# Optimization experiments

Hardware: AMD Instinct MI355X
Metric: run time of the kernel (lower is better)

Reference implementation:

```python
import jax, jax.numpy as jnp
import numpy as np

B, NQ, NK, QS, KS, H, VD = 16, 64, 512, 256, 256, 256, 256


def setup_inputs() -> dict:
    key = jax.random.key(0)
    k1, k2, k3, k4, k5, k6, k7 = jax.random.split(key, 7)
    return {
        "queries": jax.random.normal(k1, (B, NQ, QS), dtype=jnp.float32),
        "keys": jax.random.normal(k2, (B, NK, KS), dtype=jnp.float32),
        "values": jax.random.normal(k3, (B, NK, VD), dtype=jnp.float32),
        "valid_lens": jax.random.randint(k4, (B,), 1, NK + 1, dtype=jnp.int32),
        # learned params (nn.Linear with bias=False): W_q [QS,H], W_k [KS,H], w_v [H]
        "W_q": jax.random.normal(k5, (QS, H), dtype=jnp.float32) / np.sqrt(QS),
        "W_k": jax.random.normal(k6, (KS, H), dtype=jnp.float32) / np.sqrt(KS),
        "w_v": jax.random.normal(k7, (H,), dtype=jnp.float32) / np.sqrt(H),
    }


def reference(queries, keys, values, valid_lens, W_q, W_k, w_v):
    # project: q [B,nq,H], k [B,nk,H]
    q = jnp.einsum("bqd,dh->bqh", queries, W_q)
    k = jnp.einsum("bkd,dh->bkh", keys, W_k)
    # broadcast-add -> tanh -> score reduction via w_v: [B,nq,nk]
    features = jnp.tanh(q[:, :, None, :] + k[:, None, :, :])  # [B,nq,nk,H]
    scores = jnp.einsum("bqkh,h->bqk", features, w_v)
    # masked softmax over keys (positions >= valid_len masked out)
    mask = jnp.arange(scores.shape[-1])[None, None, :] < valid_lens[:, None, None]
    scores = jnp.where(mask, scores, -1e6)
    attn = jax.nn.softmax(scores, axis=-1)
    # weighted sum of values (dropout p=0 / eval mode => identity)
    return jnp.einsum("bqk,bkv->bqv", attn, values)
```

## Files before the change

### kernel.cpp

```cpp
#include <hip/hip_runtime.h>
#include <hip/hip_bf16.h>

#define BB 16
#define NQ 64
#define NK 512
#define HD 256

typedef __attribute__((ext_vector_type(8))) short short8;
typedef __attribute__((ext_vector_type(4))) float f32x4;

__device__ __forceinline__ ushort bf16_rne(float v) {
    unsigned u = __float_as_uint(v);
    return (ushort)((u + 0x7FFFu + ((u >> 16) & 1u)) >> 16);
}
__device__ __forceinline__ float bf16_to_f(ushort h) {
    return __uint_as_float(((unsigned)h) << 16);
}

__global__ __launch_bounds__(256) void wconv(
    const float* __restrict__ wq, const float* __restrict__ wk,
    ushort* __restrict__ wqh, ushort* __restrict__ wql,
    ushort* __restrict__ wkh, ushort* __restrict__ wkl)
{
    int widx = blockIdx.x * 256 + threadIdx.x;
    const float* W; ushort *wh, *wl;
    if (widx < 16384) { W = wq; wh = wqh; wl = wql; }
    else { W = wk; wh = wkh; wl = wkl; widx -= 16384; }
    int n  = widx >> 6;
    int k4 = (widx & 63) * 4;
    ushort hh[4], ll[4];
    #pragma unroll
    for (int c = 0; c < 4; ++c) {
        float v = W[(k4 + c) * 256 + n];
        hh[c] = bf16_rne(v);
        ll[c] = bf16_rne(v - bf16_to_f(hh[c]));
    }
    *(ushort4*)&wh[n * 256 + k4] = make_ushort4(hh[0], hh[1], hh[2], hh[3]);
    *(ushort4*)&wl[n * 256 + k4] = make_ushort4(ll[0], ll[1], ll[2], ll[3]);
}

__global__ __launch_bounds__(256, 2) void proj_fused(
    const float* __restrict__ queries, const float* __restrict__ keys,
    const ushort* __restrict__ wqh, const ushort* __restrict__ wql,
    const ushort* __restrict__ wkh, const ushort* __restrict__ wkl,
    float* __restrict__ qp, float* __restrict__ kp, float scale)
{
    __shared__ ushort AsH[64 * 64], AsL[64 * 64];
    __shared__ ushort BsH[64 * 64], BsL[64 * 64];

    const float* A; const ushort *Bh, *Bl; float* C; int rows0;
    const int bx = blockIdx.x;
    if (bx < 16) { A = queries; Bh = wqh; Bl = wql; C = qp; rows0 = bx * 64; }
    else         { A = keys;    Bh = wkh; Bl = wkl; C = kp; rows0 = (bx - 16) * 64; }
    const int cols0 = blockIdx.y * 64;

    const int t = threadIdx.x, lane = t & 63, wave = t >> 6;
    const int quad = lane >> 4, l15 = lane & 15;
    const int sr  = t >> 2;
    const int sc2 = (t & 3) * 2;

    f32x4 acc[4];
    #pragma unroll
    for (int j = 0; j < 4; ++j) acc[j] = (f32x4){0.f, 0.f, 0.f, 0.f};

    for (int k0 = 0; k0 < 256; k0 += 64) {
        const float* arow = &A[(size_t)(rows0 + sr) * 256 + k0 + sc2 * 8];
        float4 a0 = *(const float4*)&arow[0];
        float4 a1 = *(const float4*)&arow[4];
        float4 a2 = *(const float4*)&arow[8];
        float4 a3 = *(const float4*)&arow[12];
        const ushort* bhp = &Bh[(size_t)(cols0 + sr) * 256 + k0 + sc2 * 8];
        const ushort* blp = &Bl[(size_t)(cols0 + sr) * 256 + k0 + sc2 * 8];
        short8 b0h = *(const short8*)&bhp[0];
        short8 b1h = *(const short8*)&bhp[8];
        short8 b0l = *(const short8*)&blp[0];
        short8 b1l = *(const short8*)&blp[8];

        __syncthreads();

        float av[16] = {a0.x, a0.y, a0.z, a0.w, a1.x, a1.y, a1.z, a1.w,
                        a2.x, a2.y, a2.z, a2.w, a3.x, a3.y, a3.z, a3.w};
        short8 ah0, ah1, al0, al1;
        #pragma unroll
        for (int e = 0; e < 8; ++e) {
            ushort h0 = bf16_rne(av[e]);
            ushort h1 = bf16_rne(av[8 + e]);
            ah0[e] = (short)h0;
            ah1[e] = (short)h1;
            al0[e] = (short)bf16_rne(av[e] - bf16_to_f(h0));
            al1[e] = (short)bf16_rne(av[8 + e] - bf16_to_f(h1));
        }
        {
            int s0 = sr * 8 + ((sc2 + 0) ^ (sr & 7));
            int s1 = sr * 8 + ((sc2 + 1) ^ (sr & 7));
            *(short8*)&AsH[s0 * 8] = ah0;
            *(short8*)&AsH[s1 * 8] = ah1;
            *(short8*)&AsL[s0 * 8] = al0;
            *(short8*)&AsL[s1 * 8] = al1;
            *(short8*)&BsH[s0 * 8] = b0h;
            *(short8*)&BsH[s1 * 8] = b1h;
            *(short8*)&BsL[s0 * 8] = b0l;
            *(short8*)&BsL[s1 * 8] = b1l;
        }
        __syncthreads();

        #pragma unroll
        for (int ks = 0; ks < 2; ++ks) {
            const int c = ks * 4 + quad;
            short8 aH, aL, bH[4], bL[4];
            {
                int r = wave * 16 + l15;
                int slot = r * 8 + (c ^ (r & 7));
                aH = *(const short8*)&AsH[slot * 8];
                aL = *(const short8*)&AsL[slot * 8];
            }
            #pragma unroll
            for (int ns = 0; ns < 4; ++ns) {
                int n = ns * 16 + l15;
                int slot = n * 8 + (c ^ (n & 7));
                bH[ns] = *(const short8*)&BsH[slot * 8];
                bL[ns] = *(const short8*)&BsL[slot * 8];
            }
            #pragma unroll
            for (int ns = 0; ns < 4; ++ns)
                acc[ns] = __builtin_amdgcn_mfma_f32_16x16x32_bf16(aH, bH[ns], acc[ns], 0, 0, 0);
            #pragma unroll
            for (int ns = 0; ns < 4; ++ns)
                acc[ns] = __builtin_amdgcn_mfma_f32_16x16x32_bf16(aL, bH[ns], acc[ns], 0, 0, 0);
            #pragma unroll
            for (int ns = 0; ns < 4; ++ns)
                acc[ns] = __builtin_amdgcn_mfma_f32_16x16x32_bf16(aH, bL[ns], acc[ns], 0, 0, 0);
        }
    }

    const int rbase = rows0 + wave * 16 + quad * 4;
    #pragma unroll
    for (int ns = 0; ns < 4; ++ns) {
        int col = cols0 + ns * 16 + l15;
        #pragma unroll
        for (int r = 0; r < 4; ++r)
            C[(size_t)(rbase + r) * 256 + col] =
                __builtin_amdgcn_exp2f(acc[ns][r] * scale);
    }
}

__global__ __launch_bounds__(512, 6) void score_pv_seg5(
    const float* __restrict__ qp,
    const float* __restrict__ kp,
    const float* __restrict__ values,
    const int*   __restrict__ vlens,
    const float* __restrict__ w_v,
    float* __restrict__ pO,
    float* __restrict__ pL)
{
    __shared__ float eq[8][260];
    __shared__ float wv[HD];
    __shared__ float Ps[8][66];
    __shared__ float sP[8][66];
    __shared__ float part[4][8][260];

    const int b   = blockIdx.x & 15;
    const int qt  = blockIdx.x >> 4;
    const int seg = blockIdx.y;
    const int vl  = vlens[b];
    if (seg * 64 >= vl) return;

    const int t = threadIdx.x, lane = t & 63, wave = t >> 6;
    const int kq = wave & 3;
    const int hh = wave >> 2;
    const int key = kq * 16 + (lane >> 2);
    const int ch  = lane & 3;
    const int kg  = seg * 64 + key;

    const float* krow = kp + ((size_t)b * NK + kg) * HD + hh * 128 + ch * 4;
    float4 ek[8];
    #pragma unroll
    for (int j = 0; j < 8; ++j) ek[j] = *(const float4*)&krow[j * 16];

    const float* qsrc = qp + ((size_t)b * NQ + qt * 8) * HD;
    {
        int row = t >> 6, c4 = (t & 63) * 4;
        *(float4*)&eq[row][c4] = *(const float4*)&qsrc[(size_t)row * HD + c4];
    }
    if (t < 64) *(float4*)&wv[t * 4] = *(const float4*)&w_v[t * 4];
    __syncthreads();

    float Wsum;
    {
        float ws = wv[lane] + wv[lane + 64] + wv[lane + 128] + wv[lane + 192];
        #pragma unroll
        for (int off = 32; off; off >>= 1) ws += __shfl_xor(ws, off);
        Wsum = ws;
    }

    float s[8] = {0.f, 0.f, 0.f, 0.f, 0.f, 0.f, 0.f, 0.f};
    #pragma unroll
    for (int j = 0; j < 8; ++j) {
        const int h = hh * 128 + j * 16 + ch * 4;
        float4 e4 = ek[j];
        float4 w4 = *(const float4*)&wv[h];
        #pragma unroll
        for (int qi = 0; qi < 8; ++qi) {
            float4 q4 = *(const float4*)&eq[qi][h];
            float p0 = fmaf(q4.x, e4.x, 1.f);
            float p1 = fmaf(q4.y, e4.y, 1.f);
            float p2 = fmaf(q4.z, e4.z, 1.f);
            float p3 = fmaf(q4.w, e4.w, 1.f);
            float d01 = p0 * p1;
            float d23 = p2 * p3;
            float n01 = fmaf(w4.x, p1, w4.y * p0);
            float n23 = fmaf(w4.z, p3, w4.w * p2);
            float num = fmaf(d01, n23, d23 * n01);
            float r   = __builtin_amdgcn_rcpf(d01 * d23);
            s[qi] = fmaf(num, r, s[qi]);
        }
    }
    #pragma unroll
    for (int qi = 0; qi < 8; ++qi) {
        s[qi] += __shfl_xor(s[qi], 1);
        s[qi] += __shfl_xor(s[qi], 2);
    }
    if (hh == 1 && ch == 0) {
        #pragma unroll
        for (int qi = 0; qi < 8; ++qi) sP[qi][key] = s[qi];
    }
    __syncthreads();
    const float L2E = 1.4426950408889634f;
    if (hh == 0 && ch == 0) {
        const bool masked = (kg >= vl);
        #pragma unroll
        for (int qi = 0; qi < 8; ++qi) {
            float sv = fmaf(-2.f, s[qi] + sP[qi][key], Wsum);
            Ps[qi][key] = masked ? 0.f : __builtin_amdgcn_exp2f(sv * L2E);
        }
    }
    __syncthreads();

    const float* vbase = values + ((size_t)b * NK + seg * 64 + kq * 16) * HD;
    float4 vv[4];
    #pragma unroll
    for (int i = 0; i < 4; ++i)
        vv[i] = *(const float4*)&vbase[(size_t)i * HD + lane * 4];

    {
        float l = Ps[wave][lane];
        #pragma unroll
        for (int off = 32; off; off >>= 1) l += __shfl_xor(l, off);
        if (lane == 0)
            pL[(((size_t)(b * 8 + qt) * 8 + seg)) * 8 + wave] = l;
    }

    f32x4 acc[4];
    #pragma unroll
    for (int r = 0; r < 4; ++r) acc[r] = (f32x4){0.f, 0.f, 0.f, 0.f};
    #pragma unroll
    for (int i = 0; i < 16; ++i) {
        float4 v = vv[i & 3];
        if (i + 4 < 16)
            vv[i & 3] = *(const float4*)&vbase[(size_t)(i + 4) * HD + lane * 4];
        #pragma unroll
        for (int r = 0; r < 4; ++r) {
            float p = Ps[hh * 4 + r][kq * 16 + i];
            acc[r][0] = fmaf(p, v.x, acc[r][0]);
            acc[r][1] = fmaf(p, v.y, acc[r][1]);
            acc[r][2] = fmaf(p, v.z, acc[r][2]);
            acc[r][3] = fmaf(p, v.w, acc[r][3]);
        }
    }
    #pragma unroll
    for (int r = 0; r < 4; ++r)
        *(f32x4*)&part[kq][hh * 4 + r][lane * 4] = acc[r];
    __syncthreads();

    const size_t ob = (((size_t)(b * 8 + qt) * 8 + seg)) * 8 * 256;
    {
        int qi = t >> 6, c4 = (t & 63) * 4;
        float4 p0 = *(const float4*)&part[0][qi][c4];
        float4 p1 = *(const float4*)&part[1][qi][c4];
        float4 p2 = *(const float4*)&part[2][qi][c4];
        float4 p3 = *(const float4*)&part[3][qi][c4];
        float4 o;
        o.x = (p0.x + p1.x) + (p2.x + p3.x);
        o.y = (p0.y + p1.y) + (p2.y + p3.y);
        o.z = (p0.z + p1.z) + (p2.z + p3.z);
        o.w = (p0.w + p1.w) + (p2.w + p3.w);
        *(float4*)&pO[ob + (size_t)qi * 256 + c4] = o;
    }
}

__global__ __launch_bounds__(256) void combine_seg3(
    const float* __restrict__ pO, const float* __restrict__ pL,
    const int* __restrict__ vlens, float* __restrict__ out)
{
    const int b  = blockIdx.x >> 6;
    const int q  = blockIdx.x & 63;
    const int t  = threadIdx.x;
    const int nc = (vlens[b] + 63) >> 6;
    const int qt = q >> 3, qi = q & 7;

    const size_t base = (size_t)(b * 8 + qt) * 8;

    float L = 0.f, acc = 0.f;
    #pragma unroll
    for (int i = 0; i < 8; ++i) {
        if (i < nc) {
            L   += pL[(base + i) * 8 + qi];
            acc += pO[((base + i) * 8 + qi) * 256 + t];
        }
    }
    out[((size_t)(b * 64 + q)) * 256 + t] = acc * __builtin_amdgcn_rcpf(L);
}

extern "C" void kernel_launch(void* const* d_in, const int* in_sizes, int n_in,
                              void* d_out, int out_size, void* d_ws, size_t ws_size,
                              hipStream_t stream) {
    const float* queries = (const float*)d_in[0];
    const float* keys    = (const float*)d_in[1];
    const float* values  = (const float*)d_in[2];
    const int*   vlens   = (const int*)d_in[3];
    const float* W_q     = (const float*)d_in[4];
    const float* W_k     = (const float*)d_in[5];
    const float* w_v     = (const float*)d_in[6];
    float* out = (float*)d_out;

    float*  kp  = (float*)d_ws;
    float*  qp  = kp + (size_t)BB * NK * HD;
    float*  pO  = qp + (size_t)BB * NQ * HD;
    float*  pL  = pO + (size_t)BB * 8 * 8 * 8 * 256;
    ushort* wqh = (ushort*)(pL + (size_t)BB * 8 * 8 * 8);
    ushort* wql = wqh + 65536;
    ushort* wkh = wql + 65536;
    ushort* wkl = wkh + 65536;

    const float SC = 2.885390081777927f;

    wconv<<<dim3(128), 256, 0, stream>>>(W_q, W_k, wqh, wql, wkh, wkl);
    proj_fused<<<dim3(144, 4), 256, 0, stream>>>(queries, keys,
                                                 wqh, wql, wkh, wkl,
                                                 qp, kp, SC);
    score_pv_seg5<<<dim3(128, 8), 512, 0, stream>>>(qp, kp, values, vlens, w_v,
                                                    pO, pL);
    combine_seg3<<<dim3(BB * NQ), 256, 0, stream>>>(pO, pL, vlens, out);
}
```

Baseline: 110.4 us.

## Fuse score, PV and combine into one kernel looping over key segments

Replaces the split-K score/PV kernel plus the separate combine kernel with a single kernel. Each block owns one batch and four queries and loops over the valid 64-key segments, prefetching the next segment's keys and values into registers while computing the current one, with double-buffered P in shared memory. This removes the partial-output round trip through global memory and one launch. The cost is less parallelism (256 blocks instead of up to 1024) and a serial dependence on each batch's valid length, so load balance across blocks may suffer.

Result: slower. 114.4 us (+3.6%).

```diff
diff --git a/kernel.cpp b/kernel.cpp
--- a/kernel.cpp
+++ b/kernel.cpp
@@ -16,6 +16,12 @@
 __device__ __forceinline__ float bf16_to_f(ushort h) {
     return __uint_as_float(((unsigned)h) << 16);
 }
+
+#define BARRIER_LGKM() do { \
+    asm volatile("s_waitcnt lgkmcnt(0)" ::: "memory"); \
+    __builtin_amdgcn_s_barrier(); \
+    asm volatile("" ::: "memory"); \
+} while (0)
 
 __global__ __launch_bounds__(256) void wconv(
     const float* __restrict__ wq, const float* __restrict__ wk,
@@ -144,46 +150,53 @@
     }
 }
 
-__global__ __launch_bounds__(512, 6) void score_pv_seg5(
+__global__ __launch_bounds__(512) void score_fused(
     const float* __restrict__ qp,
     const float* __restrict__ kp,
     const float* __restrict__ values,
     const int*   __restrict__ vlens,
     const float* __restrict__ w_v,
-    float* __restrict__ pO,
-    float* __restrict__ pL)
+    float* __restrict__ out)
 {
-    __shared__ float eq[8][260];
+    __shared__ float eq[4][260];
     __shared__ float wv[HD];
-    __shared__ float Ps[8][66];
-    __shared__ float sP[8][66];
-    __shared__ float part[4][8][260];
-
-    const int b   = blockIdx.x & 15;
-    const int qt  = blockIdx.x >> 4;
-    const int seg = blockIdx.y;
-    const int vl  = vlens[b];
-    if (seg * 64 >= vl) return;
+    __shared__ float Ps[2][4][66];
+    __shared__ float part[8][4][260];
+    __shared__ float Lbuf[8][4];
+
+    const int b  = blockIdx.x;
+    const int qt = blockIdx.y;
+    const int vl = vlens[b];
+    const int nc = (vl + 63) >> 6;
 
     const int t = threadIdx.x, lane = t & 63, wave = t >> 6;
-    const int kq = wave & 3;
-    const int hh = wave >> 2;
-    const int key = kq * 16 + (lane >> 2);
-    const int ch  = lane & 3;
-    const int kg  = seg * 64 + key;
-
-    const float* krow = kp + ((size_t)b * NK + kg) * HD + hh * 128 + ch * 4;
-    float4 ek[8];
-    #pragma unroll
-    for (int j = 0; j < 8; ++j) ek[j] = *(const float4*)&krow[j * 16];
-
-    const float* qsrc = qp + ((size_t)b * NQ + qt * 8) * HD;
+    const int key8 = lane >> 3;
+    const int ch8  = lane & 7;
+    const int wkey = wave * 8 + key8;
+    const float L2E = 1.4426950408889634f;
+
+    const float* kbase = kp + (size_t)b * NK * HD;
+    const float* vbase = values + (size_t)b * NK * HD;
+
+    float4 ekA[8], ekB[8], vv[8];
     {
+        const float* kr = kbase + (size_t)wkey * HD + ch8 * 4;
+        #pragma unroll
+        for (int j = 0; j < 8; ++j) ekA[j] = *(const float4*)&kr[j * 32];
+        #pragma unroll
+        for (int i = 0; i < 8; ++i)
+            vv[i] = *(const float4*)&vbase[(size_t)(wave * 8 + i) * HD + lane * 4];
+    }
+
+    const float* qsrc = qp + ((size_t)b * NQ + qt * 4) * HD;
+    if (t < 256) {
         int row = t >> 6, c4 = (t & 63) * 4;
         *(float4*)&eq[row][c4] = *(const float4*)&qsrc[(size_t)row * HD + c4];
-    }
-    if (t < 64) *(float4*)&wv[t * 4] = *(const float4*)&w_v[t * 4];
-    __syncthreads();
+    } else if (t < 320) {
+        int i = t - 256;
+        *(float4*)&wv[i * 4] = *(const float4*)&w_v[i * 4];
+    }
+    BARRIER_LGKM();
 
     float Wsum;
     {
@@ -193,122 +206,103 @@
         Wsum = ws;
     }
 
-    float s[8] = {0.f, 0.f, 0.f, 0.f, 0.f, 0.f, 0.f, 0.f};
-    #pragma unroll
-    for (int j = 0; j < 8; ++j) {
-        const int h = hh * 128 + j * 16 + ch * 4;
-        float4 e4 = ek[j];
-        float4 w4 = *(const float4*)&wv[h];
-        #pragma unroll
-        for (int qi = 0; qi < 8; ++qi) {
-            float4 q4 = *(const float4*)&eq[qi][h];
-            float p0 = fmaf(q4.x, e4.x, 1.f);
-            float p1 = fmaf(q4.y, e4.y, 1.f);
-            float p2 = fmaf(q4.z, e4.z, 1.f);
-            float p3 = fmaf(q4.w, e4.w, 1.f);
-            float d01 = p0 * p1;
-            float d23 = p2 * p3;
-            float n01 = fmaf(w4.x, p1, w4.y * p0);
-            float n23 = fmaf(w4.z, p3, w4.w * p2);
-            float num = fmaf(d01, n23, d23 * n01);
-            float r   = __builtin_amdgcn_rcpf(d01 * d23);
-            s[qi] = fmaf(num, r, s[qi]);
+    f32x4 acc[4];
+    #pragma unroll
+    for (int qi = 0; qi < 4; ++qi) acc[qi] = (f32x4){0.f, 0.f, 0.f, 0.f};
+    float Lacc[4] = {0.f, 0.f, 0.f, 0.f};
+
+#define SEG_STEP(EKCUR, EKNXT)                                               \
+    {                                                                        \
+        if (seg + 1 < nc) {                                                  \
+            const float* kr = kbase + (size_t)((seg + 1) * 64 + wkey) * HD + ch8 * 4; \
+            _Pragma("unroll")                                                \
+            for (int j = 0; j < 8; ++j) EKNXT[j] = *(const float4*)&kr[j * 32]; \
+        }                                                                    \
+        float sA[4] = {0.f, 0.f, 0.f, 0.f};                                  \
+        _Pragma("unroll")                                                    \
+        for (int j = 0; j < 8; ++j) {                                        \
+            const int h = j * 32 + ch8 * 4;                                  \
+            float4 e4 = EKCUR[j];                                            \
+            float4 w4 = *(const float4*)&wv[h];                              \
+            _Pragma("unroll")                                                \
+            for (int qi = 0; qi < 4; ++qi) {                                 \
+                float4 q4 = *(const float4*)&eq[qi][h];                      \
+                float p0 = fmaf(q4.x, e4.x, 1.f);                            \
+                float p1 = fmaf(q4.y, e4.y, 1.f);                            \
+                float p2 = fmaf(q4.z, e4.z, 1.f);                            \
+                float p3 = fmaf(q4.w, e4.w, 1.f);                            \
+                float d01 = p0 * p1, d23 = p2 * p3;                          \
+                float n01 = fmaf(w4.x, p1, w4.y * p0);                       \
+                float n23 = fmaf(w4.z, p3, w4.w * p2);                       \
+                float num = fmaf(d01, n23, d23 * n01);                       \
+                float r   = __builtin_amdgcn_rcpf(d01 * d23);                \
+                sA[qi] = fmaf(num, r, sA[qi]);                               \
+            }                                                                \
+        }                                                                    \
+        _Pragma("unroll")                                                    \
+        for (int qi = 0; qi < 4; ++qi) {                                     \
+            sA[qi] += __shfl_xor(sA[qi], 1);                                 \
+            sA[qi] += __shfl_xor(sA[qi], 2);                                 \
+            sA[qi] += __shfl_xor(sA[qi], 4);                                 \
+        }                                                                    \
+        const bool masked = (seg * 64 + wkey >= vl);                         \
+        const int pb = seg & 1;                                              \
+        _Pragma("unroll")                                                    \
+        for (int qi = 0; qi < 4; ++qi) {                                     \
+            float sv = fmaf(-2.f, sA[qi], Wsum);                             \
+            float e  = masked ? 0.f : __builtin_amdgcn_exp2f(sv * L2E);      \
+            Lacc[qi] += e;                                                   \
+            if (ch8 == 0) Ps[pb][qi][wkey] = e;                              \
+        }                                                                    \
+        BARRIER_LGKM();                                                      \
+        _Pragma("unroll")                                                    \
+        for (int i = 0; i < 8; ++i) {                                        \
+            float4 v = vv[i];                                                \
+            if (seg + 1 < nc)                                                \
+                vv[i] = *(const float4*)&vbase[(size_t)((seg + 1) * 64 + wave * 8 + i) * HD + lane * 4]; \
+            _Pragma("unroll")                                                \
+            for (int qi = 0; qi < 4; ++qi) {                                 \
+                float p = Ps[pb][qi][wave * 8 + i];                          \
+                acc[qi][0] = fmaf(p, v.x, acc[qi][0]);                       \
+                acc[qi][1] = fmaf(p, v.y, acc[qi][1]);                       \
+                acc[qi][2] = fmaf(p, v.z, acc[qi][2]);                       \
+                acc[qi][3] = fmaf(p, v.w, acc[qi][3]);                       \
+            }                                                                \
+        }                                                                    \
+    }
+
+    int seg = 0;
+    while (true) {
+        SEG_STEP(ekA, ekB)
+        if (++seg >= nc) break;
+        SEG_STEP(ekB, ekA)
+        if (++seg >= nc) break;
+    }
+#undef SEG_STEP
+
+    #pragma unroll
+    for (int qi = 0; qi < 4; ++qi) {
+        float l = Lacc[qi];
+        #pragma unroll
+        for (int off = 32; off; off >>= 1) l += __shfl_xor(l, off);
+        if (lane == 0) Lbuf[wave][qi] = l * 0.125f;
+        *(f32x4*)&part[wave][qi][lane * 4] = acc[qi];
+    }
+    BARRIER_LGKM();
+
+    if (t < 256) {
+        int qi = t >> 6, c4 = (t & 63) * 4;
+        float ox = 0.f, oy = 0.f, oz = 0.f, ow = 0.f, L = 0.f;
+        #pragma unroll
+        for (int w = 0; w < 8; ++w) {
+            float4 p = *(const float4*)&part[w][qi][c4];
+            ox += p.x; oy += p.y; oz += p.z; ow += p.w;
+            L += Lbuf[w][qi];
         }
-    }
-    #pragma unroll
-    for (int qi = 0; qi < 8; ++qi) {
-        s[qi] += __shfl_xor(s[qi], 1);
-        s[qi] += __shfl_xor(s[qi], 2);
-    }
-    if (hh == 1 && ch == 0) {
-        #pragma unroll
-        for (int qi = 0; qi < 8; ++qi) sP[qi][key] = s[qi];
-    }
-    __syncthreads();
-    const float L2E = 1.4426950408889634f;
-    if (hh == 0 && ch == 0) {
-        const bool masked = (kg >= vl);
-        #pragma unroll
-        for (int qi = 0; qi < 8; ++qi) {
-            float sv = fmaf(-2.f, s[qi] + sP[qi][key], Wsum);
-            Ps[qi][key] = masked ? 0.f : __builtin_amdgcn_exp2f(sv * L2E);
-        }
-    }
-    __syncthreads();
-
-    const float* vbase = values + ((size_t)b * NK + seg * 64 + kq * 16) * HD;
-    float4 vv[4];
-    #pragma unroll
-    for (int i = 0; i < 4; ++i)
-        vv[i] = *(const float4*)&vbase[(size_t)i * HD + lane * 4];
-
-    {
-        float l = Ps[wave][lane];
-        #pragma unroll
-        for (int off = 32; off; off >>= 1) l += __shfl_xor(l, off);
-        if (lane == 0)
-            pL[(((size_t)(b * 8 + qt) * 8 + seg)) * 8 + wave] = l;
-    }
-
-    f32x4 acc[4];
-    #pragma unroll
-    for (int r = 0; r < 4; ++r) acc[r] = (f32x4){0.f, 0.f, 0.f, 0.f};
-    #pragma unroll
-    for (int i = 0; i < 16; ++i) {
-        float4 v = vv[i & 3];
-        if (i + 4 < 16)
-            vv[i & 3] = *(const float4*)&vbase[(size_t)(i + 4) * HD + lane * 4];
-        #pragma unroll
-        for (int r = 0; r < 4; ++r) {
-            float p = Ps[hh * 4 + r][kq * 16 + i];
-            acc[r][0] = fmaf(p, v.x, acc[r][0]);
-            acc[r][1] = fmaf(p, v.y, acc[r][1]);
-            acc[r][2] = fmaf(p, v.z, acc[r][2]);
-            acc[r][3] = fmaf(p, v.w, acc[r][3]);
-        }
-    }
-    #pragma unroll
-    for (int r = 0; r < 4; ++r)
-        *(f32x4*)&part[kq][hh * 4 + r][lane * 4] = acc[r];
-    __syncthreads();
-
-    const size_t ob = (((size_t)(b * 8 + qt) * 8 + seg)) * 8 * 256;
-    {
-        int qi = t >> 6, c4 = (t & 63) * 4;
-        float4 p0 = *(const float4*)&part[0][qi][c4];
-        float4 p1 = *(const float4*)&part[1][qi][c4];
-        float4 p2 = *(const float4*)&part[2][qi][c4];
-        float4 p3 = *(const float4*)&part[3][qi][c4];
-        float4 o;
-        o.x = (p0.x + p1.x) + (p2.x + p3.x);
-        o.y = (p0.y + p1.y) + (p2.y + p3.y);
-        o.z = (p0.z + p1.z) + (p2.z + p3.z);
-        o.w = (p0.w + p1.w) + (p2.w + p3.w);
-        *(float4*)&pO[ob + (size_t)qi * 256 + c4] = o;
-    }
-}
-
-__global__ __launch_bounds__(256) void combine_seg3(
-    const float* __restrict__ pO, const float* __restrict__ pL,
-    const int* __restrict__ vlens, float* __restrict__ out)
-{
-    const int b  = blockIdx.x >> 6;
-    const int q  = blockIdx.x & 63;
-    const int t  = threadIdx.x;
-    const int nc = (vlens[b] + 63) >> 6;
-    const int qt = q >> 3, qi = q & 7;
-
-    const size_t base = (size_t)(b * 8 + qt) * 8;
-
-    float L = 0.f, acc = 0.f;
-    #pragma unroll
-    for (int i = 0; i < 8; ++i) {
-        if (i < nc) {
-            L   += pL[(base + i) * 8 + qi];
-            acc += pO[((base + i) * 8 + qi) * 256 + t];
-        }
-    }
-    out[((size_t)(b * 64 + q)) * 256 + t] = acc * __builtin_amdgcn_rcpf(L);
+        float r = __builtin_amdgcn_rcpf(L);
+        float4 o = make_float4(ox * r, oy * r, oz * r, ow * r);
+        *(float4*)&out[((size_t)(b * NQ + qt * 4 + qi)) * 256 + c4] = o;
+    }
 }
 
 extern "C" void kernel_launch(void* const* d_in, const int* in_sizes, int n_in,
@@ -325,9 +319,7 @@
 
     float*  kp  = (float*)d_ws;
     float*  qp  = kp + (size_t)BB * NK * HD;
-    float*  pO  = qp + (size_t)BB * NQ * HD;
-    float*  pL  = pO + (size_t)BB * 8 * 8 * 8 * 256;
-    ushort* wqh = (ushort*)(pL + (size_t)BB * 8 * 8 * 8);
+    ushort* wqh = (ushort*)(qp + (size_t)BB * NQ * HD);
     ushort* wql = wqh + 65536;
     ushort* wkh = wql + 65536;
     ushort* wkl = wkh + 65536;
@@ -338,7 +330,6 @@
     proj_fused<<<dim3(144, 4), 256, 0, stream>>>(queries, keys,
                                                  wqh, wql, wkh, wkl,
                                                  qp, kp, SC);
-    score_pv_seg5<<<dim3(128, 8), 512, 0, stream>>>(qp, kp, values, vlens, w_v,
-                                                    pO, pL);
-    combine_seg3<<<dim3(BB * NQ), 256, 0, stream>>>(pO, pL, vlens, out);
-}
+    score_fused<<<dim3(16, 16), 512, 0, stream>>>(qp, kp, values, vlens, w_v,
+                                                  out);
+}
```
